# Optimization experiments

Hardware: AMD Instinct MI355X
Metric: run time of the kernel (lower is better)

The kernel has to match this reference:

```python
import jax, jax.numpy as jnp
import numpy as np

GROUP_SIZE = 64
OUT_FEATURES = 4096
IN_FEATURES = 4096
NUM_GROUPS = IN_FEATURES // GROUP_SIZE


def setup_inputs() -> dict:
    key = jax.random.key(0)
    k1, k2, k3, k4, k5 = jax.random.split(key, 5)
    x = jax.random.normal(k1, (4, 2048, IN_FEATURES), dtype=jnp.float32)
    # Packed bytes: two 4-bit nibbles per byte (uint8 semantics, stored as int32).
    weight_packed = jax.random.randint(k2, (OUT_FEATURES * NUM_GROUPS, GROUP_SIZE // 2), 0, 256, dtype=jnp.int32)
    # Per-group affine params; small scales keep dequantized weights realistic.
    weight_scales = jax.random.uniform(k3, (OUT_FEATURES * NUM_GROUPS,), dtype=jnp.float32) * 0.01 + 1e-4
    weight_zeros = jax.random.normal(k4, (OUT_FEATURES * NUM_GROUPS,), dtype=jnp.float32) * 0.05
    bias = jax.random.normal(k5, (OUT_FEATURES,), dtype=jnp.float32) * 0.02
    return {"x": x, "weight_packed": weight_packed, "weight_scales": weight_scales,
            "weight_zeros": weight_zeros, "bias": bias}


def _dequantize_4bit(packed, scales, zeros):
    # packed: [G, group_size//2] ints in [0,256). low nibble -> even slots, high -> odd.
    low = (packed & 15).astype(jnp.float32)
    high = ((packed >> 4) & 15).astype(jnp.float32)
    g = packed.shape[0]
    unpacked = jnp.stack([low, high], axis=-1).reshape(g, GROUP_SIZE)  # interleave
    deq = unpacked * scales[:, None] + zeros[:, None]
    return deq.reshape(OUT_FEATURES, IN_FEATURES)


def reference(x, weight_packed, weight_scales, weight_zeros, bias):
    weight = _dequantize_4bit(weight_packed, weight_scales, weight_zeros)  # [O, I]
    # F.linear: x @ weight.T + bias
    out = jnp.einsum('bsi,oi->bso', x, weight) + bias
    return out
```

## Files before the change

kernel.cpp:

```cpp
#include <hip/hip_runtime.h>
#include <hip/hip_bf16.h>


typedef short short8 __attribute__((ext_vector_type(8)));
typedef float float4v __attribute__((ext_vector_type(4)));
typedef int int4v __attribute__((ext_vector_type(4)));

#define M_TOTAL 8192
#define N_OUT 4096
#define K_IN 4096
#define BM 256
#define BN 256
#define BK 64
#define NT (K_IN / BK)

__device__ __forceinline__ short f2bf(float f) {
  unsigned int u = __builtin_bit_cast(unsigned int, f);
  unsigned int r = (u + 0x7fffu + ((u >> 16) & 1u)) >> 16;
  return (short)(unsigned short)r;
}

__device__ __forceinline__ void gload_lds16(const void* g, void* l) {
  __builtin_amdgcn_global_load_lds(
      (const __attribute__((address_space(1))) void*)g,
      (__attribute__((address_space(3))) void*)l, 16, 0, 0);
}

__global__ __launch_bounds__(256)
void cvt_x_kernel(const float* __restrict__ x, short* __restrict__ xb, int n8) {
  int i = blockIdx.x * blockDim.x + threadIdx.x;
  int stride = gridDim.x * blockDim.x;
  for (; i < n8; i += stride) {
    const float* p = x + (size_t)i * 8;
    float4v f0 = *reinterpret_cast<const float4v*>(p);
    float4v f1 = *reinterpret_cast<const float4v*>(p + 4);
    short8 v;
#pragma unroll
    for (int e = 0; e < 4; ++e) { v[e] = f2bf(f0[e]); v[4 + e] = f2bf(f1[e]); }
    *reinterpret_cast<short8*>(xb + (size_t)i * 8) = v;
  }
}

__global__ __launch_bounds__(256)
void deq_w_kernel(const int* __restrict__ wp, const float* __restrict__ wsc,
                  const float* __restrict__ wzr, short* __restrict__ wb) {
  int t = blockIdx.x * blockDim.x + threadIdx.x;
  int g = t >> 1, h = t & 1;
  float s = wsc[g], z = wzr[g];
  const int* p = wp + (size_t)g * 32 + h * 16;
  int4v b[4];
#pragma unroll
  for (int u = 0; u < 4; ++u) b[u] = *reinterpret_cast<const int4v*>(p + u * 4);
  short* o = wb + (size_t)t * 32;
#pragma unroll
  for (int u = 0; u < 4; ++u) {
    short8 v;
#pragma unroll
    for (int e = 0; e < 4; ++e) {
      int bb = b[u][e];
      v[2 * e]     = f2bf((float)(bb & 15) * s + z);
      v[2 * e + 1] = f2bf((float)((bb >> 4) & 15) * s + z);
    }
    *reinterpret_cast<short8*>(o + u * 8) = v;
  }
}

#define MFMA_BF16 __builtin_amdgcn_mfma_f32_16x16x32_bf16
#define BAR() __builtin_amdgcn_s_barrier()
#define PRIO1() __builtin_amdgcn_s_setprio(1)
#define PRIO0() __builtin_amdgcn_s_setprio(0)
#define VMCNT6() asm volatile("s_waitcnt vmcnt(6)" ::: "memory")
#define VMCNT0() asm volatile("s_waitcnt vmcnt(0)" ::: "memory")

__global__ __launch_bounds__(512, 2)
void qgemm8_kernel(const short* __restrict__ A, const short* __restrict__ B,
                   const float* __restrict__ bias, float* __restrict__ out) {
  __shared__ __align__(16) char L[131072];

  const int tid  = threadIdx.x;
  const int lane = tid & 63;
  const int w    = tid >> 6;
  const int wm   = w >> 2;
  const int wn   = w & 3;

  const int id  = blockIdx.x;
  const int xcd = id & 7;
  const int s   = id >> 3;
  const int by  = (s >> 5) * 16 + 2 * xcd + ((s & 31) >> 4);
  const int bx  = s & 15;
  const int m0  = by * BM;
  const int o0  = bx * BN;

  const int kslot = (lane & 7) ^ ((lane >> 3) & 7);
  const int R0 = w * 16 + (lane >> 3);
  const int R1 = R0 + 8;
  const short* pA0 = A + (size_t)(m0 + (R0 >> 6) * 128 + (R0 & 63)) * K_IN + kslot * 8;
  const short* pA1 = A + (size_t)(m0 + (R1 >> 6) * 128 + (R1 & 63)) * K_IN + kslot * 8;
  const short* pB0 = B + (size_t)(o0 + (R0 >> 5) * 64 + (R0 & 31)) * K_IN + kslot * 8;
  const short* pB1 = B + (size_t)(o0 + (R1 >> 5) * 64 + (R1 & 31)) * K_IN + kslot * 8;
  const int ldsp0 = w * 2048 + lane * 16;
  const int ldsp1 = ldsp0 + 1024;

#define STAGE_A(buf, mg, t) do { \
    gload_lds16(pA0 + (size_t)(mg) * 64 * K_IN + (t) * 64, &L[(buf) * 65536 + (mg) * 16384 + ldsp0]); \
    gload_lds16(pA1 + (size_t)(mg) * 64 * K_IN + (t) * 64, &L[(buf) * 65536 + (mg) * 16384 + ldsp1]); \
  } while (0)
#define STAGE_B(buf, ng, t) do { \
    gload_lds16(pB0 + (size_t)(ng) * 32 * K_IN + (t) * 64, &L[(buf) * 65536 + 32768 + (ng) * 16384 + ldsp0]); \
    gload_lds16(pB1 + (size_t)(ng) * 32 * K_IN + (t) * 64, &L[(buf) * 65536 + 32768 + (ng) * 16384 + ldsp1]); \
  } while (0)

  const int l15   = lane & 15;
  const int abase = wm * 8192 + l15 * 128;
  const int bbase = 32768 + wn * 4096 + l15 * 128;
  const int sl0 = (((lane >> 4) + 0) ^ (lane & 7)) * 16;
  const int sl1 = (((lane >> 4) + 4) ^ (lane & 7)) * 16;

  short8 a[8], bl[4], br[4];

#define RD_A(buf, mg) do { \
    _Pragma("unroll") for (int mf = 0; mf < 4; ++mf) { \
      a[mf * 2 + 0] = *reinterpret_cast<const short8*>(&L[(buf) * 65536 + (mg) * 16384 + abase + mf * 2048 + sl0]); \
      a[mf * 2 + 1] = *reinterpret_cast<const short8*>(&L[(buf) * 65536 + (mg) * 16384 + abase + mf * 2048 + sl1]); \
    } } while (0)
#define RD_B(dst, buf, ng) do { \
    _Pragma("unroll") for (int nf = 0; nf < 2; ++nf) { \
      dst[nf * 2 + 0] = *reinterpret_cast<const short8*>(&L[(buf) * 65536 + (ng) * 16384 + bbase + nf * 2048 + sl0]); \
      dst[nf * 2 + 1] = *reinterpret_cast<const short8*>(&L[(buf) * 65536 + (ng) * 16384 + bbase + nf * 2048 + sl1]); \
    } } while (0)

  float4v acc[8][4];
#pragma unroll
  for (int i = 0; i < 8; ++i)
#pragma unroll
    for (int j = 0; j < 4; ++j) acc[i][j] = (float4v){0.f, 0.f, 0.f, 0.f};

#define DO_QUAD(mg, ng, bb_) do { \
    _Pragma("unroll") for (int ks = 0; ks < 2; ++ks) \
    _Pragma("unroll") for (int mf = 0; mf < 4; ++mf) \
    _Pragma("unroll") for (int nf = 0; nf < 2; ++nf) \
      acc[(mg) * 4 + mf][(ng) * 2 + nf] = \
        MFMA_BF16(a[mf * 2 + ks], bb_[nf * 2 + ks], acc[(mg) * 4 + mf][(ng) * 2 + nf], 0, 0, 0); \
  } while (0)

  STAGE_A(0, 0, 0); STAGE_B(0, 1, 0); STAGE_B(0, 0, 0); STAGE_A(0, 1, 0);
  STAGE_A(1, 0, 1); STAGE_B(1, 1, 1); STAGE_B(1, 0, 1);
  VMCNT6();
  BAR();

  for (int i = 0; i < NT / 2 - 1; ++i) {
    const int t2 = 2 * i + 2, t3 = 2 * i + 3;
    RD_A(0, 0); RD_B(br, 0, 1);
    STAGE_A(1, 1, t3 - 2);
    BAR(); PRIO1(); DO_QUAD(0, 1, br); PRIO0(); BAR();
    RD_B(bl, 0, 0);
    STAGE_A(0, 0, t2);
    BAR(); PRIO1(); DO_QUAD(0, 0, bl); PRIO0(); BAR();
    RD_A(0, 1);
    STAGE_B(0, 1, t2);
    BAR(); PRIO1(); DO_QUAD(1, 0, bl); PRIO0(); BAR();
    STAGE_B(0, 0, t2);
    VMCNT6();
    BAR(); PRIO1(); DO_QUAD(1, 1, br); PRIO0(); BAR();
    RD_A(1, 0); RD_B(br, 1, 1);
    STAGE_A(0, 1, t2);
    BAR(); PRIO1(); DO_QUAD(0, 1, br); PRIO0(); BAR();
    RD_B(bl, 1, 0);
    STAGE_A(1, 0, t3);
    BAR(); PRIO1(); DO_QUAD(0, 0, bl); PRIO0(); BAR();
    RD_A(1, 1);
    STAGE_B(1, 1, t3);
    BAR(); PRIO1(); DO_QUAD(1, 0, bl); PRIO0(); BAR();
    STAGE_B(1, 0, t3);
    VMCNT6();
    BAR(); PRIO1(); DO_QUAD(1, 1, br); PRIO0(); BAR();
  }

  RD_A(0, 0); RD_B(br, 0, 1);
  STAGE_A(1, 1, 63);
  BAR(); PRIO1(); DO_QUAD(0, 1, br); PRIO0(); BAR();
  RD_B(bl, 0, 0);
  BAR(); PRIO1(); DO_QUAD(0, 0, bl); PRIO0(); BAR();
  RD_A(0, 1);
  BAR(); PRIO1(); DO_QUAD(1, 0, bl); PRIO0(); BAR();
  VMCNT0();
  BAR(); PRIO1(); DO_QUAD(1, 1, br); PRIO0(); BAR();
  RD_A(1, 0); RD_B(br, 1, 1);
  BAR(); PRIO1(); DO_QUAD(0, 1, br); PRIO0(); BAR();
  RD_B(bl, 1, 0);
  BAR(); PRIO1(); DO_QUAD(0, 0, bl); PRIO0(); BAR();
  RD_A(1, 1);
  BAR(); PRIO1(); DO_QUAD(1, 0, bl); PRIO0(); BAR();
  PRIO1(); DO_QUAD(1, 1, br); PRIO0();

#pragma unroll
  for (int nf = 0; nf < 4; ++nf) {
    const int col = o0 + wn * 64 + nf * 16 + l15;
    const float bb = bias[col];
#pragma unroll
    for (int mf = 0; mf < 8; ++mf) {
      const int rowb = m0 + wm * 128 + mf * 16 + (lane >> 4) * 4;
#pragma unroll
      for (int r = 0; r < 4; ++r)
        out[(size_t)(rowb + r) * N_OUT + col] = acc[mf][nf][r] + bb;
    }
  }
}

extern "C" void kernel_launch(void* const* d_in, const int* in_sizes, int n_in,
                              void* d_out, int out_size, void* d_ws, size_t ws_size,
                              hipStream_t stream) {
  const float* x    = (const float*)d_in[0];
  const int* wp     = (const int*)d_in[1];
  const float* wsc  = (const float*)d_in[2];
  const float* wzr  = (const float*)d_in[3];
  const float* bias = (const float*)d_in[4];
  float* out = (float*)d_out;

  const size_t xb_bytes = (size_t)M_TOTAL * K_IN * 2;
  short* xb = (short*)d_ws;
  short* wb = (short*)((char*)d_ws + xb_bytes);

  cvt_x_kernel<<<2048, 256, 0, stream>>>(x, xb, (int)((size_t)M_TOTAL * K_IN / 8));
  deq_w_kernel<<<2048, 256, 0, stream>>>(wp, wsc, wzr, wb);
  qgemm8_kernel<<<dim3(512), dim3(512), 0, stream>>>(xb, wb, bias, out);
}
```

Measured before the change: 274.3 us.

## Restructure GEMM main loop into half-tile phases with fewer barriers

The main loop of the bf16 MFMA GEMM is reorganised from eight single-quadrant phases per iteration, each bracketed by two barriers, into four phases that each compute two quadrants after one barrier. B fragments for both halves are read up front, global-to-LDS stages are batched, and the vmcnt waits are retuned (8, then 2 and 0 in the tail). The aim is less barrier and synchronisation overhead and longer uninterrupted MFMA runs. In exchange, register pressure rises, the overlap of loads with compute changes, and any mistake in the waitcnt accounting could cause LDS read/write races.

After: 271.6 us. Within noise of the previous version (-1.0%).

```diff
diff --git a/kernel.cpp b/kernel.cpp
--- a/kernel.cpp
+++ b/kernel.cpp
@@ -69,7 +69,8 @@
 #define BAR() __builtin_amdgcn_s_barrier()
 #define PRIO1() __builtin_amdgcn_s_setprio(1)
 #define PRIO0() __builtin_amdgcn_s_setprio(0)
-#define VMCNT6() asm volatile("s_waitcnt vmcnt(6)" ::: "memory")
+#define VMCNT8() asm volatile("s_waitcnt vmcnt(8)" ::: "memory")
+#define VMCNT2() asm volatile("s_waitcnt vmcnt(2)" ::: "memory")
 #define VMCNT0() asm volatile("s_waitcnt vmcnt(0)" ::: "memory")
 
 __global__ __launch_bounds__(512, 2)
@@ -145,53 +146,41 @@
 
   STAGE_A(0, 0, 0); STAGE_B(0, 1, 0); STAGE_B(0, 0, 0); STAGE_A(0, 1, 0);
   STAGE_A(1, 0, 1); STAGE_B(1, 1, 1); STAGE_B(1, 0, 1);
-  VMCNT6();
+  VMCNT8();
   BAR();
 
   for (int i = 0; i < NT / 2 - 1; ++i) {
     const int t2 = 2 * i + 2, t3 = 2 * i + 3;
-    RD_A(0, 0); RD_B(br, 0, 1);
+    RD_A(0, 0); RD_B(br, 0, 1); RD_B(bl, 0, 0);
     STAGE_A(1, 1, t3 - 2);
-    BAR(); PRIO1(); DO_QUAD(0, 1, br); PRIO0(); BAR();
-    RD_B(bl, 0, 0);
-    STAGE_A(0, 0, t2);
-    BAR(); PRIO1(); DO_QUAD(0, 0, bl); PRIO0(); BAR();
+    PRIO1(); DO_QUAD(0, 1, br); DO_QUAD(0, 0, bl); PRIO0();
+    VMCNT8(); BAR();
     RD_A(0, 1);
-    STAGE_B(0, 1, t2);
-    BAR(); PRIO1(); DO_QUAD(1, 0, bl); PRIO0(); BAR();
-    STAGE_B(0, 0, t2);
-    VMCNT6();
-    BAR(); PRIO1(); DO_QUAD(1, 1, br); PRIO0(); BAR();
-    RD_A(1, 0); RD_B(br, 1, 1);
+    STAGE_A(0, 0, t2); STAGE_B(0, 1, t2); STAGE_B(0, 0, t2);
+    PRIO1(); DO_QUAD(1, 0, bl); DO_QUAD(1, 1, br); PRIO0();
+    VMCNT8(); BAR();
+    RD_A(1, 0); RD_B(br, 1, 1); RD_B(bl, 1, 0);
     STAGE_A(0, 1, t2);
-    BAR(); PRIO1(); DO_QUAD(0, 1, br); PRIO0(); BAR();
-    RD_B(bl, 1, 0);
-    STAGE_A(1, 0, t3);
-    BAR(); PRIO1(); DO_QUAD(0, 0, bl); PRIO0(); BAR();
+    PRIO1(); DO_QUAD(0, 1, br); DO_QUAD(0, 0, bl); PRIO0();
+    VMCNT8(); BAR();
     RD_A(1, 1);
-    STAGE_B(1, 1, t3);
-    BAR(); PRIO1(); DO_QUAD(1, 0, bl); PRIO0(); BAR();
-    STAGE_B(1, 0, t3);
-    VMCNT6();
-    BAR(); PRIO1(); DO_QUAD(1, 1, br); PRIO0(); BAR();
-  }
-
-  RD_A(0, 0); RD_B(br, 0, 1);
+    STAGE_A(1, 0, t3); STAGE_B(1, 1, t3); STAGE_B(1, 0, t3);
+    PRIO1(); DO_QUAD(1, 0, bl); DO_QUAD(1, 1, br); PRIO0();
+    VMCNT8(); BAR();
+  }
+
+  RD_A(0, 0); RD_B(br, 0, 1); RD_B(bl, 0, 0);
   STAGE_A(1, 1, 63);
-  BAR(); PRIO1(); DO_QUAD(0, 1, br); PRIO0(); BAR();
-  RD_B(bl, 0, 0);
-  BAR(); PRIO1(); DO_QUAD(0, 0, bl); PRIO0(); BAR();
+  PRIO1(); DO_QUAD(0, 1, br); DO_QUAD(0, 0, bl); PRIO0();
+  VMCNT8(); BAR();
   RD_A(0, 1);
-  BAR(); PRIO1(); DO_QUAD(1, 0, bl); PRIO0(); BAR();
-  VMCNT0();
-  BAR(); PRIO1(); DO_QUAD(1, 1, br); PRIO0(); BAR();
-  RD_A(1, 0); RD_B(br, 1, 1);
-  BAR(); PRIO1(); DO_QUAD(0, 1, br); PRIO0(); BAR();
-  RD_B(bl, 1, 0);
-  BAR(); PRIO1(); DO_QUAD(0, 0, bl); PRIO0(); BAR();
+  PRIO1(); DO_QUAD(1, 0, bl); DO_QUAD(1, 1, br); PRIO0();
+  VMCNT2(); BAR();
+  RD_A(1, 0); RD_B(br, 1, 1); RD_B(bl, 1, 0);
+  PRIO1(); DO_QUAD(0, 1, br); DO_QUAD(0, 0, bl); PRIO0();
+  VMCNT0(); BAR();
   RD_A(1, 1);
-  BAR(); PRIO1(); DO_QUAD(1, 0, bl); PRIO0(); BAR();
-  PRIO1(); DO_QUAD(1, 1, br); PRIO0();
+  PRIO1(); DO_QUAD(1, 0, bl); DO_QUAD(1, 1, br); PRIO0();
 
 #pragma unroll
   for (int nf = 0; nf < 4; ++nf) {
```
